# Optimization experiments

Hardware: AMD Instinct MI355X
Metric: run time of the kernel (lower is better)

## Reference

```python
import jax, jax.numpy as jnp
import numpy as np

N_NODES = 100000
N_EDGES = 1600000


def setup_inputs() -> dict:
    key = jax.random.key(0)
    ks = jax.random.split(key, 12)
    inp = {
        "x": jax.random.normal(ks[0], (N_NODES, 8), dtype=jnp.float32),
        "edge_index": jax.random.randint(ks[1], (2, N_EDGES), 0, N_NODES, dtype=jnp.int32),
        "W1_l": jax.random.normal(ks[2], (8, 64), dtype=jnp.float32) * 0.1,
        "b1": jax.random.normal(ks[3], (64,), dtype=jnp.float32) * 0.1,
        "W1_r": jax.random.normal(ks[4], (8, 64), dtype=jnp.float32) * 0.1,
        "W2_l": jax.random.normal(ks[5], (64, 64), dtype=jnp.float32) * 0.1,
        "b2": jax.random.normal(ks[6], (64,), dtype=jnp.float32) * 0.1,
        "W2_r": jax.random.normal(ks[7], (64, 64), dtype=jnp.float32) * 0.1,
        "fc1_W": jax.random.normal(ks[8], (64, 64), dtype=jnp.float32) * 0.1,
        "fc1_b": jax.random.normal(ks[9], (64,), dtype=jnp.float32) * 0.1,
        "fc2_W": jax.random.normal(ks[10], (64, 10), dtype=jnp.float32) * 0.1,
        "fc2_b": jax.random.normal(ks[11], (10,), dtype=jnp.float32) * 0.1,
    }
    return inp


def _sage_conv(x, edge_index, W_l, b_l, W_r, num_nodes):
    """PyG SAGEConv (mean aggr): lin_l(mean_j x_j) + lin_r(x_i)."""
    src, dst = edge_index[0], edge_index[1]
    msg = x[src]  # (E, F) gather
    summed = jax.ops.segment_sum(msg, dst, num_segments=num_nodes)  # (N, F)
    deg = jax.ops.segment_sum(jnp.ones((edge_index.shape[1],), dtype=x.dtype), dst,
                              num_segments=num_nodes)
    mean = summed / jnp.maximum(deg, 1.0)[:, None]
    return mean @ W_l + b_l + x @ W_r


def reference(x, edge_index, W1_l, b1, W1_r, W2_l, b2, W2_r, fc1_W, fc1_b, fc2_W, fc2_b):
    n = x.shape[0]
    h = jax.nn.relu(_sage_conv(x, edge_index, W1_l, b1, W1_r, n))
    h = jax.nn.relu(_sage_conv(h, edge_index, W2_l, b2, W2_r, n))
    # global_mean_pool with all-zero batch ids == mean over all nodes -> (1, 64)
    g = jnp.mean(h, axis=0, keepdims=True)
    a = jax.nn.relu(g @ fc1_W + fc1_b)
    a = a @ fc2_W + fc2_b
    return jax.nn.softmax(a, axis=-1)
```

## Files before the change

### kernel.cpp

```cpp
#include <hip/hip_runtime.h>
#include <hip/hip_bf16.h>
#include <hip/hip_fp16.h>

#define N_NODES 100000
#define N_EDGES 1600000
#define NBUCK ((N_NODES + 255) >> 8)
#define CAP 8192
#define NQ (N_NODES / 4)

typedef _Float16 f16x2 __attribute__((ext_vector_type(2)));

__device__ inline float2 h2_to_f2(unsigned int u) {
    __half2 h = *reinterpret_cast<__half2*>(&u);
    return __half22float2(h);
}
__device__ inline f16x2 uf2(unsigned int u) {
    union { unsigned int u; f16x2 h; } v;
    v.u = u;
    return v.h;
}
#if __has_builtin(__builtin_amdgcn_fdot2)
#define DOT2(a, b, c) __builtin_amdgcn_fdot2((a), (b), (c), false)
#else
__device__ inline float DOT2(f16x2 a, f16x2 b, float c) {
    return c + (float)a.x * (float)b.x + (float)a.y * (float)b.y;
}
#endif

__global__ void k_zero(int* __restrict__ p, int n) {
    for (int i = threadIdx.x; i < n; i += 256) p[i] = 0;
}

__global__ __launch_bounds__(256) void k_stage(const int* __restrict__ src,
                                               const int* __restrict__ dst,
                                               int* __restrict__ bcursor,
                                               unsigned int* __restrict__ stage) {
    __shared__ int h[NBUCK];
    __shared__ int base[NBUCK];
    __shared__ int cur[NBUCK];
    const int epb = (N_EDGES + gridDim.x - 1) / gridDim.x;
    const int c0 = blockIdx.x * epb;
    const int c1 = (c0 + epb < N_EDGES) ? (c0 + epb) : N_EDGES;

    for (int i = threadIdx.x; i < NBUCK; i += 256) { h[i] = 0; cur[i] = 0; }
    __syncthreads();
    for (int e = c0 + threadIdx.x; e < c1; e += 256)
        atomicAdd(&h[dst[e] >> 8], 1);
    __syncthreads();
    for (int i = threadIdx.x; i < NBUCK; i += 256)
        base[i] = h[i] ? atomicAdd(&bcursor[i], h[i]) : 0;
    __syncthreads();
    for (int e = c0 + threadIdx.x; e < c1; e += 256) {
        int d = dst[e];
        int b = d >> 8;
        int pos = base[b] + atomicAdd(&cur[b], 1);
        if (pos < CAP)
            stage[b * CAP + pos] = ((unsigned int)(d & 255) << 17) | (unsigned int)src[e];
    }
}

__global__ __launch_bounds__(512) void k_bsort(unsigned int* __restrict__ stage,
                                               const int* __restrict__ bcursor,
                                               int* __restrict__ row_start,
                                               int* __restrict__ deg) {
    __shared__ int off[256];
    __shared__ int cur[256];
    __shared__ unsigned int out[CAP];
    const int b = blockIdx.x;
    int cnt = bcursor[b];
    if (cnt > CAP) cnt = CAP;
    const int s = b * CAP;
    const int tid = threadIdx.x;

    if (tid < 256) cur[tid] = 0;
    __syncthreads();
    for (int i = tid; i < cnt; i += 512)
        atomicAdd(&cur[stage[s + i] >> 17], 1);
    __syncthreads();
    int v = 0;
    if (tid < 256) {
        v = cur[tid];
        off[tid] = v;
    }
    __syncthreads();
    for (int d = 1; d < 256; d <<= 1) {
        int t = 0;
        if (tid < 256 && tid >= d) t = off[tid - d];
        __syncthreads();
        if (tid < 256) off[tid] += t;
        __syncthreads();
    }
    if (tid < 256) {
        int ex = off[tid] - v;
        off[tid] = ex;
        cur[tid] = 0;
        int node = b * 256 + tid;
        if (node < N_NODES) {
            row_start[node] = s + ex;
            deg[node] = v;
        }
    }
    __syncthreads();

    for (int i = tid; i < cnt; i += 512) {
        unsigned int p = stage[s + i];
        int l = p >> 17;
        int pos = off[l] + atomicAdd(&cur[l], 1);
        out[pos] = p & 0x1FFFFu;
    }
    __syncthreads();
    for (int i = tid; i < cnt; i += 512)
        stage[s + i] = out[i];
}

__global__ __launch_bounds__(256) void layer1(
    const float* __restrict__ x, const int* __restrict__ row_start,
    const int* __restrict__ deg, const int* __restrict__ csr,
    const float* __restrict__ W1l, const float* __restrict__ b1,
    const float* __restrict__ W1r, __half* __restrict__ h1h) {
    const int lane = threadIdx.x & 63;
    const int g = lane >> 3;
    const int sub = lane & 7;

    float wl1[8], wr1[8];
#pragma unroll
    for (int k = 0; k < 8; k++) {
        wl1[k] = W1l[k * 64 + lane];
        wr1[k] = W1r[k * 64 + lane];
    }
    float bv = b1[lane];
    asm volatile("" ::: "memory");

    const int gwid = (blockIdx.x * blockDim.x + threadIdx.x) >> 6;
    const int nwaves = (gridDim.x * blockDim.x) >> 6;

    for (int node = gwid; node < N_NODES; node += nwaves) {
        int rs = row_start[node];
        int dg = deg[node];
        int re = rs + dg;
        float acc = 0.0f;
        int t = rs;
        for (; t + 16 <= re; t += 16) {
            int i0 = csr[t + g];
            int i1 = csr[t + 8 + g];
            acc += x[i0 * 8 + sub] + x[i1 * 8 + sub];
        }
        for (; t + 8 <= re; t += 8) {
            int i0 = csr[t + g];
            acc += x[i0 * 8 + sub];
        }
        int r = re - t;
        if (r > 0) {
            int ii = csr[(t + g < re) ? (t + g) : (re - 1)];
            float v = x[ii * 8 + sub];
            if (g < r) acc += v;
        }
        acc += __shfl_xor(acc, 8);
        acc += __shfl_xor(acc, 16);
        acc += __shfl_xor(acc, 32);
        float inv = 1.0f / fmaxf((float)dg, 1.0f);
        float mean = acc * inv;
        float xself = x[node * 8 + sub];
        float m[8], xk[8];
#pragma unroll
        for (int k = 0; k < 8; k++) {
            m[k]  = __shfl(mean, k);
            xk[k] = __shfl(xself, k);
        }
        float a = bv;
#pragma unroll
        for (int k = 0; k < 8; k++)
            a += m[k] * wl1[k] + xk[k] * wr1[k];
        h1h[node * 64 + lane] = __float2half(fmaxf(a, 0.0f));
    }
}

__global__ __launch_bounds__(256) void agg2(
    const __half* __restrict__ h1h, const int* __restrict__ row_start,
    const int* __restrict__ deg, const int* __restrict__ csr,
    __half* __restrict__ mean2h) {
    const int lane = threadIdx.x & 63;
    const int g = lane >> 4;
    const int sub = lane & 15;

    const int gwid = (blockIdx.x * blockDim.x + threadIdx.x) >> 6;
    const int nwaves = (gridDim.x * blockDim.x) >> 6;

    for (int node = gwid; node < N_NODES; node += nwaves) {
        int rs = row_start[node];
        int dg = deg[node];
        int re = rs + dg;
        float4 acc = {0.f, 0.f, 0.f, 0.f};
        int t = rs;
        for (; t + 8 <= re; t += 8) {
            int i0 = csr[t + g];
            int i1 = csr[t + 4 + g];
            uint2 a = *(const uint2*)(h1h + i0 * 64 + sub * 4);
            uint2 b = *(const uint2*)(h1h + i1 * 64 + sub * 4);
            float2 a0 = h2_to_f2(a.x), a1 = h2_to_f2(a.y);
            float2 b0 = h2_to_f2(b.x), b1 = h2_to_f2(b.y);
            acc.x += a0.x + b0.x; acc.y += a0.y + b0.y;
            acc.z += a1.x + b1.x; acc.w += a1.y + b1.y;
        }
        for (; t + 4 <= re; t += 4) {
            int i0 = csr[t + g];
            uint2 a = *(const uint2*)(h1h + i0 * 64 + sub * 4);
            float2 a0 = h2_to_f2(a.x), a1 = h2_to_f2(a.y);
            acc.x += a0.x; acc.y += a0.y; acc.z += a1.x; acc.w += a1.y;
        }
        int r = re - t;
        if (r > 0) {
            int ii = csr[(t + g < re) ? (t + g) : (re - 1)];
            uint2 a = *(const uint2*)(h1h + ii * 64 + sub * 4);
            if (g < r) {
                float2 a0 = h2_to_f2(a.x), a1 = h2_to_f2(a.y);
                acc.x += a0.x; acc.y += a0.y; acc.z += a1.x; acc.w += a1.y;
            }
        }
#pragma unroll
        for (int m = 16; m <= 32; m <<= 1) {
            acc.x += __shfl_xor(acc.x, m);
            acc.y += __shfl_xor(acc.y, m);
            acc.z += __shfl_xor(acc.z, m);
            acc.w += __shfl_xor(acc.w, m);
        }
        float inv = 1.0f / fmaxf((float)dg, 1.0f);
        if (lane < 16) {
            __half2 o0 = __floats2half2_rn(acc.x * inv, acc.y * inv);
            __half2 o1 = __floats2half2_rn(acc.z * inv, acc.w * inv);
            uint2 pk;
            pk.x = *(unsigned int*)&o0;
            pk.y = *(unsigned int*)&o1;
            *(uint2*)(mean2h + node * 64 + sub * 4) = pk;
        }
    }
}

__global__ __launch_bounds__(256) void mlp2(
    const __half* __restrict__ mean2h, const __half* __restrict__ h1h,
    const float* __restrict__ W2l, const float* __restrict__ b2,
    const float* __restrict__ W2r, float* __restrict__ gsum) {
    __shared__ __align__(16) unsigned short sh[4][2][512];
    __shared__ float part[4][64];
    const int tid = threadIdx.x;
    const int lane = tid & 63;
    const int w = tid >> 6;

    f16x2 w2[64];
#pragma unroll
    for (int k2 = 0; k2 < 32; k2++) {
        f16x2 t;
        t.x = (_Float16)W2l[(2 * k2) * 64 + lane];
        t.y = (_Float16)W2l[(2 * k2 + 1) * 64 + lane];
        w2[k2] = t;
        f16x2 u;
        u.x = (_Float16)W2r[(2 * k2) * 64 + lane];
        u.y = (_Float16)W2r[(2 * k2 + 1) * 64 + lane];
        w2[32 + k2] = u;
    }
    float bv = b2[lane];
    asm volatile("" ::: "memory");

    const int n = lane >> 4;
    const int r = (lane >> 3) & 1;
    const int c = lane & 7;
    const __half* sbase = r ? h1h : mean2h;

    const int gwid = (blockIdx.x * blockDim.x + tid) >> 6;
    const int nwaves = (gridDim.x * blockDim.x) >> 6;
    float pool = 0.0f;

    int q = gwid;
    uint4 cur = {0, 0, 0, 0};
    if (q < NQ)
        cur = *(const uint4*)(sbase + (size_t)(q * 4 + n) * 64 + c * 8);
    int p = 0;
    while (q < NQ) {
        *(uint4*)&sh[w][p][lane * 8] = cur;
        int qn = q + nwaves;
        uint4 nxt = {0, 0, 0, 0};
        if (qn < NQ)
            nxt = *(const uint4*)(sbase + (size_t)(qn * 4 + n) * 64 + c * 8);
        const uint4* rows = (const uint4*)&sh[w][p][0];
        float a0 = bv, a1 = bv, a2 = bv, a3 = bv;
#pragma unroll
        for (int cc = 0; cc < 16; cc++) {
            uint4 r0 = rows[cc];
            uint4 r1 = rows[16 + cc];
            uint4 r2 = rows[32 + cc];
            uint4 r3 = rows[48 + cc];
            f16x2 wa = w2[cc * 4 + 0], wb = w2[cc * 4 + 1];
            f16x2 wc = w2[cc * 4 + 2], wd = w2[cc * 4 + 3];
            a0 = DOT2(uf2(r0.x), wa, a0); a0 = DOT2(uf2(r0.y), wb, a0);
            a0 = DOT2(uf2(r0.z), wc, a0); a0 = DOT2(uf2(r0.w), wd, a0);
            a1 = DOT2(uf2(r1.x), wa, a1); a1 = DOT2(uf2(r1.y), wb, a1);
            a1 = DOT2(uf2(r1.z), wc, a1); a1 = DOT2(uf2(r1.w), wd, a1);
            a2 = DOT2(uf2(r2.x), wa, a2); a2 = DOT2(uf2(r2.y), wb, a2);
            a2 = DOT2(uf2(r2.z), wc, a2); a2 = DOT2(uf2(r2.w), wd, a2);
            a3 = DOT2(uf2(r3.x), wa, a3); a3 = DOT2(uf2(r3.y), wb, a3);
            a3 = DOT2(uf2(r3.z), wc, a3); a3 = DOT2(uf2(r3.w), wd, a3);
        }
        pool += fmaxf(a0, 0.0f) + fmaxf(a1, 0.0f) +
                fmaxf(a2, 0.0f) + fmaxf(a3, 0.0f);
        cur = nxt;
        p ^= 1;
        q = qn;
    }

    part[w][lane] = pool;
    __syncthreads();
    if (tid < 64)
        atomicAdd(&gsum[tid],
                  part[0][tid] + part[1][tid] + part[2][tid] + part[3][tid]);
}

__global__ void head(const float* __restrict__ gsum,
                     const float* __restrict__ fc1W, const float* __restrict__ fc1b,
                     const float* __restrict__ fc2W, const float* __restrict__ fc2b,
                     float* __restrict__ out) {
    __shared__ float g[64];
    __shared__ float a1[64];
    __shared__ float a2[10];
    int j = threadIdx.x;
    g[j] = gsum[j] * (1.0f / (float)N_NODES);
    __syncthreads();
    float acc = fc1b[j];
    for (int k = 0; k < 64; k++) acc += g[k] * fc1W[k * 64 + j];
    a1[j] = fmaxf(acc, 0.0f);
    __syncthreads();
    if (j < 10) {
        float acc2 = fc2b[j];
        for (int k = 0; k < 64; k++) acc2 += a1[k] * fc2W[k * 10 + j];
        a2[j] = acc2;
    }
    __syncthreads();
    if (j == 0) {
        float mx = -1e30f;
        for (int i = 0; i < 10; i++) mx = fmaxf(mx, a2[i]);
        float s = 0.0f;
        float e[10];
        for (int i = 0; i < 10; i++) {
            e[i] = expf(a2[i] - mx);
            s += e[i];
        }
        float invs = 1.0f / s;
        for (int i = 0; i < 10; i++) out[i] = e[i] * invs;
    }
}

extern "C" void kernel_launch(void* const* d_in, const int* in_sizes, int n_in,
                              void* d_out, int out_size, void* d_ws, size_t ws_size,
                              hipStream_t stream) {
    const float* x    = (const float*)d_in[0];
    const int*   ei   = (const int*)d_in[1];
    const float* W1l  = (const float*)d_in[2];
    const float* b1   = (const float*)d_in[3];
    const float* W1r  = (const float*)d_in[4];
    const float* W2l  = (const float*)d_in[5];
    const float* b2   = (const float*)d_in[6];
    const float* W2r  = (const float*)d_in[7];
    const float* fc1W = (const float*)d_in[8];
    const float* fc1b = (const float*)d_in[9];
    const float* fc2W = (const float*)d_in[10];
    const float* fc2b = (const float*)d_in[11];
    float* out = (float*)d_out;

    const int* src = ei;
    const int* dst = ei + N_EDGES;

    __half* h1h    = (__half*)d_ws;
    unsigned int* stage = (unsigned int*)(h1h + (size_t)N_NODES * 64);
    int* csr       = (int*)stage;
    __half* mean2h = (__half*)(stage + (size_t)NBUCK * CAP);
    int* row_start = (int*)(mean2h + (size_t)N_NODES * 64);
    int* deg       = row_start + N_NODES;
    int* bcursor   = deg + N_NODES;
    float* gsum    = (float*)(bcursor + NBUCK);

    k_zero<<<1, 256, 0, stream>>>(bcursor, NBUCK + 64);

    k_stage<<<512, 256, 0, stream>>>(src, dst, bcursor, stage);
    k_bsort<<<NBUCK, 512, 0, stream>>>(stage, bcursor, row_start, deg);
    layer1<<<2048, 256, 0, stream>>>(x, row_start, deg, csr, W1l, b1, W1r, h1h);
    agg2<<<2048, 256, 0, stream>>>(h1h, row_start, deg, csr, mean2h);
    mlp2<<<512, 256, 0, stream>>>(mean2h, h1h, W2l, b2, W2r, gsum);
    head<<<1, 64, 0, stream>>>(gsum, fc1W, fc1b, fc2W, fc2b, out);
}
```

Measured before the change: 143.8 us.

## Use MFMA 16x16x32 f16 instructions for layer-2 linear and pooling

After: 132.4 us. 7.9% less time.

```diff
diff --git a/kernel.cpp b/kernel.cpp
--- a/kernel.cpp
+++ b/kernel.cpp
@@ -6,26 +6,15 @@
 #define N_EDGES 1600000
 #define NBUCK ((N_NODES + 255) >> 8)
 #define CAP 8192
-#define NQ (N_NODES / 4)
-
-typedef _Float16 f16x2 __attribute__((ext_vector_type(2)));
+#define NMT (N_NODES / 16)
+
+typedef _Float16 f16x8 __attribute__((ext_vector_type(8)));
+typedef float f32x4 __attribute__((ext_vector_type(4)));
 
 __device__ inline float2 h2_to_f2(unsigned int u) {
     __half2 h = *reinterpret_cast<__half2*>(&u);
     return __half22float2(h);
 }
-__device__ inline f16x2 uf2(unsigned int u) {
-    union { unsigned int u; f16x2 h; } v;
-    v.u = u;
-    return v.h;
-}
-#if __has_builtin(__builtin_amdgcn_fdot2)
-#define DOT2(a, b, c) __builtin_amdgcn_fdot2((a), (b), (c), false)
-#else
-__device__ inline float DOT2(f16x2 a, f16x2 b, float c) {
-    return c + (float)a.x * (float)b.x + (float)a.y * (float)b.y;
-}
-#endif
 
 __global__ void k_zero(int* __restrict__ p, int n) {
     for (int i = threadIdx.x; i < n; i += 256) p[i] = 0;
@@ -236,78 +225,71 @@
     }
 }
 
-__global__ __launch_bounds__(256) void mlp2(
+__global__ __launch_bounds__(256) void mlp2_mfma(
     const __half* __restrict__ mean2h, const __half* __restrict__ h1h,
     const float* __restrict__ W2l, const float* __restrict__ b2,
     const float* __restrict__ W2r, float* __restrict__ gsum) {
-    __shared__ __align__(16) unsigned short sh[4][2][512];
     __shared__ float part[4][64];
     const int tid = threadIdx.x;
     const int lane = tid & 63;
     const int w = tid >> 6;
-
-    f16x2 w2[64];
-#pragma unroll
-    for (int k2 = 0; k2 < 32; k2++) {
-        f16x2 t;
-        t.x = (_Float16)W2l[(2 * k2) * 64 + lane];
-        t.y = (_Float16)W2l[(2 * k2 + 1) * 64 + lane];
-        w2[k2] = t;
-        f16x2 u;
-        u.x = (_Float16)W2r[(2 * k2) * 64 + lane];
-        u.y = (_Float16)W2r[(2 * k2 + 1) * 64 + lane];
-        w2[32 + k2] = u;
-    }
-    float bv = b2[lane];
+    const int row16 = lane & 15;
+    const int grp = lane >> 4;
+
+    f16x8 bf[4][4];
+#pragma unroll
+    for (int c = 0; c < 4; c++) {
+        const float* Wsrc = (c < 2) ? W2l : W2r;
+        int koff = (c & 1) * 32 + grp * 8;
+#pragma unroll
+        for (int nt = 0; nt < 4; nt++) {
+            f16x8 t;
+#pragma unroll
+            for (int j = 0; j < 8; j++)
+                t[j] = (_Float16)Wsrc[(koff + j) * 64 + nt * 16 + row16];
+            bf[c][nt] = t;
+        }
+    }
+    float bv[4];
+#pragma unroll
+    for (int nt = 0; nt < 4; nt++) bv[nt] = b2[nt * 16 + row16];
     asm volatile("" ::: "memory");
-
-    const int n = lane >> 4;
-    const int r = (lane >> 3) & 1;
-    const int c = lane & 7;
-    const __half* sbase = r ? h1h : mean2h;
 
     const int gwid = (blockIdx.x * blockDim.x + tid) >> 6;
     const int nwaves = (gridDim.x * blockDim.x) >> 6;
-    float pool = 0.0f;
-
-    int q = gwid;
-    uint4 cur = {0, 0, 0, 0};
-    if (q < NQ)
-        cur = *(const uint4*)(sbase + (size_t)(q * 4 + n) * 64 + c * 8);
-    int p = 0;
-    while (q < NQ) {
-        *(uint4*)&sh[w][p][lane * 8] = cur;
-        int qn = q + nwaves;
-        uint4 nxt = {0, 0, 0, 0};
-        if (qn < NQ)
-            nxt = *(const uint4*)(sbase + (size_t)(qn * 4 + n) * 64 + c * 8);
-        const uint4* rows = (const uint4*)&sh[w][p][0];
-        float a0 = bv, a1 = bv, a2 = bv, a3 = bv;
-#pragma unroll
-        for (int cc = 0; cc < 16; cc++) {
-            uint4 r0 = rows[cc];
-            uint4 r1 = rows[16 + cc];
-            uint4 r2 = rows[32 + cc];
-            uint4 r3 = rows[48 + cc];
-            f16x2 wa = w2[cc * 4 + 0], wb = w2[cc * 4 + 1];
-            f16x2 wc = w2[cc * 4 + 2], wd = w2[cc * 4 + 3];
-            a0 = DOT2(uf2(r0.x), wa, a0); a0 = DOT2(uf2(r0.y), wb, a0);
-            a0 = DOT2(uf2(r0.z), wc, a0); a0 = DOT2(uf2(r0.w), wd, a0);
-            a1 = DOT2(uf2(r1.x), wa, a1); a1 = DOT2(uf2(r1.y), wb, a1);
-            a1 = DOT2(uf2(r1.z), wc, a1); a1 = DOT2(uf2(r1.w), wd, a1);
-            a2 = DOT2(uf2(r2.x), wa, a2); a2 = DOT2(uf2(r2.y), wb, a2);
-            a2 = DOT2(uf2(r2.z), wc, a2); a2 = DOT2(uf2(r2.w), wd, a2);
-            a3 = DOT2(uf2(r3.x), wa, a3); a3 = DOT2(uf2(r3.y), wb, a3);
-            a3 = DOT2(uf2(r3.z), wc, a3); a3 = DOT2(uf2(r3.w), wd, a3);
-        }
-        pool += fmaxf(a0, 0.0f) + fmaxf(a1, 0.0f) +
-                fmaxf(a2, 0.0f) + fmaxf(a3, 0.0f);
-        cur = nxt;
-        p ^= 1;
-        q = qn;
-    }
-
-    part[w][lane] = pool;
+    float pool[4] = {0.f, 0.f, 0.f, 0.f};
+
+    for (int mt = gwid; mt < NMT; mt += nwaves) {
+        int n0 = mt * 16;
+        const __half* am = mean2h + (size_t)(n0 + row16) * 64 + grp * 8;
+        const __half* ah = h1h    + (size_t)(n0 + row16) * 64 + grp * 8;
+        f16x8 af[4];
+        af[0] = *(const f16x8*)(am);
+        af[1] = *(const f16x8*)(am + 32);
+        af[2] = *(const f16x8*)(ah);
+        af[3] = *(const f16x8*)(ah + 32);
+#pragma unroll
+        for (int nt = 0; nt < 4; nt++) {
+            f32x4 acc = {bv[nt], bv[nt], bv[nt], bv[nt]};
+#pragma unroll
+            for (int c = 0; c < 4; c++)
+                acc = __builtin_amdgcn_mfma_f32_16x16x32_f16(af[c], bf[c][nt],
+                                                             acc, 0, 0, 0);
+            pool[nt] += fmaxf(acc[0], 0.f) + fmaxf(acc[1], 0.f) +
+                        fmaxf(acc[2], 0.f) + fmaxf(acc[3], 0.f);
+        }
+    }
+
+#pragma unroll
+    for (int nt = 0; nt < 4; nt++) {
+        pool[nt] += __shfl_xor(pool[nt], 16);
+        pool[nt] += __shfl_xor(pool[nt], 32);
+    }
+    if (lane < 16) {
+#pragma unroll
+        for (int nt = 0; nt < 4; nt++)
+            part[w][nt * 16 + row16] = pool[nt];
+    }
     __syncthreads();
     if (tid < 64)
         atomicAdd(&gsum[tid],
@@ -383,6 +365,6 @@
     k_bsort<<<NBUCK, 512, 0, stream>>>(stage, bcursor, row_start, deg);
     layer1<<<2048, 256, 0, stream>>>(x, row_start, deg, csr, W1l, b1, W1r, h1h);
     agg2<<<2048, 256, 0, stream>>>(h1h, row_start, deg, csr, mean2h);
-    mlp2<<<512, 256, 0, stream>>>(mean2h, h1h, W2l, b2, W2r, gsum);
+    mlp2_mfma<<<512, 256, 0, stream>>>(mean2h, h1h, W2l, b2, W2r, gsum);
     head<<<1, 64, 0, stream>>>(gsum, fc1W, fc1b, fc2W, fc2b, out);
 }
```
